# Kernel tuning notes

Measured on AMD Instinct MI355X. Metric: run time of the kernel, lower is better.

Reference implementation:

```python
import jax, jax.numpy as jnp
import numpy as np

ATT_SCALE = 1.0

def setup_inputs() -> dict:
    key = jax.random.key(0)
    ks = jax.random.split(key, 9)
    N, Cin, Cout, E = 50000, 512, 512, 400000
    x = jax.random.normal(ks[0], (N, Cin), dtype=jnp.float32)
    eb = jax.random.randint(ks[1], (2, E), 0, N, dtype=jnp.int32)
    ev = jax.random.randint(ks[2], (2, E), 0, N, dtype=jnp.int32)
    ec = jax.random.randint(ks[3], (2, E), 0, N, dtype=jnp.int32)
    s = 1.0 / np.sqrt(Cin)
    W_bond = jax.random.normal(ks[4], (Cout, Cin), dtype=jnp.float32) * s
    W_vin = jax.random.normal(ks[5], (Cout, Cin), dtype=jnp.float32) * s
    W_vconn = jax.random.normal(ks[6], (Cout, Cin), dtype=jnp.float32) * s
    att_proj = jax.random.normal(ks[7], (Cout,), dtype=jnp.float32)
    bias = jnp.zeros((Cout,), dtype=jnp.float32)
    return {"x": x, "edge_index_bond": eb, "edge_index_virtual_intra": ev,
            "edge_index_virtual_conn": ec, "W_bond": W_bond, "W_vin": W_vin,
            "W_vconn": W_vconn, "att_proj": att_proj, "bias": bias}

def reference(x, edge_index_bond, edge_index_virtual_intra, edge_index_virtual_conn,
              W_bond, W_vin, W_vconn, att_proj, bias):
    N = x.shape[0]
    x_bond = x @ W_bond.T    # [N, Cout]
    x_vin = x @ W_vin.T
    x_vconn = x @ W_vconn.T

    # --- bond edges: add self loops, symmetric degree normalization ---
    loops = jnp.arange(N, dtype=edge_index_bond.dtype)
    row = jnp.concatenate([edge_index_bond[0], loops])
    col = jnp.concatenate([edge_index_bond[1], loops])
    deg = jax.ops.segment_sum(jnp.ones_like(row, dtype=x_bond.dtype), row, num_segments=N)
    dinv = jnp.where(deg > 0, deg ** -0.5, 0.0)
    norm = dinv[row] * dinv[col]                       # [E+N]
    out = jax.ops.segment_sum(x_bond[col] * norm[:, None], row, num_segments=N)

    # --- virtual intra edges: mean aggregation ---
    row_v, col_v = edge_index_virtual_intra[0], edge_index_virtual_intra[1]
    sum_vin = jax.ops.segment_sum(x_vin[col_v], row_v, num_segments=N)
    deg_vin = jnp.clip(jax.ops.segment_sum(jnp.ones_like(row_v, dtype=x_vin.dtype), row_v, num_segments=N), 1.0)
    out = out + sum_vin / deg_vin[:, None]

    # --- virtual conn edges: sigmoid dot-product attention ---
    row_c, col_c = edge_index_virtual_conn[0], edge_index_virtual_conn[1]
    proj_i = x_vconn[row_c] * att_proj
    proj_j = x_vconn[col_c] * att_proj
    alpha = jax.nn.sigmoid(jnp.sum(proj_i * proj_j, axis=-1) * ATT_SCALE)  # [E]
    out = out + jax.ops.segment_sum(alpha[:, None] * x_vconn[col_c], row_c, num_segments=N)

    return out + bias
```

## Files before the change

kernel.cpp:

```cpp
#include <hip/hip_runtime.h>
#include <hip/hip_fp8.h>
#include <stdint.h>

typedef _Float16 f16x8 __attribute__((ext_vector_type(8)));
typedef _Float16 f16x2 __attribute__((ext_vector_type(2)));
typedef float f32x4 __attribute__((ext_vector_type(4)));
typedef float f32x2 __attribute__((ext_vector_type(2)));

__device__ __forceinline__ unsigned short f2h(float f) {
    _Float16 h = (_Float16)f;
    return __builtin_bit_cast(unsigned short, h);
}
__device__ __forceinline__ float h2f(unsigned short s) {
    _Float16 h = __builtin_bit_cast(_Float16, s);
    return (float)h;
}

__device__ __forceinline__ unsigned pack_q4(float f0, float f1, float f2, float f3) {
#if __has_builtin(__builtin_amdgcn_cvt_pk_fp8_f32)
    unsigned u = (unsigned)__builtin_amdgcn_cvt_pk_fp8_f32(f0, f1, 0, false);
    u = (unsigned)__builtin_amdgcn_cvt_pk_fp8_f32(f2, f3, u, true);
    return u;
#else
    __hip_fp8_e4m3 q0(f0), q1(f1), q2(f2), q3(f3);
    return (unsigned)q0.__x | ((unsigned)q1.__x << 8) |
           ((unsigned)q2.__x << 16) | ((unsigned)q3.__x << 24);
#endif
}
__device__ __forceinline__ void add_q8(float* a, uint2 v, float s) {
#if __has_builtin(__builtin_amdgcn_cvt_pk_f32_fp8)
    f32x2 p0 = __builtin_amdgcn_cvt_pk_f32_fp8(v.x, false);
    f32x2 p1 = __builtin_amdgcn_cvt_pk_f32_fp8(v.x, true);
    f32x2 p2 = __builtin_amdgcn_cvt_pk_f32_fp8(v.y, false);
    f32x2 p3 = __builtin_amdgcn_cvt_pk_f32_fp8(v.y, true);
    a[0] += s * p0[0]; a[1] += s * p0[1];
    a[2] += s * p1[0]; a[3] += s * p1[1];
    a[4] += s * p2[0]; a[5] += s * p2[1];
    a[6] += s * p3[0]; a[7] += s * p3[1];
#else
    unsigned char b[8];
    *(uint2*)b = v;
    #pragma unroll
    for (int j = 0; j < 8; j++) {
        __hip_fp8_e4m3 q; q.__x = b[j];
        a[j] += s * (float)q;
    }
#endif
}

__device__ __forceinline__ void gload16(const void* g, void* lds) {
    __builtin_amdgcn_global_load_lds(
        (const __attribute__((address_space(1))) void*)g,
        (__attribute__((address_space(3))) void*)lds, 16, 0, 0);
}

#if __has_builtin(__builtin_amdgcn_fdot2)
__device__ __forceinline__ float dot2(f16x2 a, f16x2 b, float c) {
    return __builtin_amdgcn_fdot2(a, b, c, false);
}
#else
__device__ __forceinline__ float dot2(f16x2 a, f16x2 b, float c) {
    return c + (float)a[0] * (float)b[0] + (float)a[1] * (float)b[1];
}
#endif

__global__ __launch_bounds__(256) void k_prep(
    const float* __restrict__ x, unsigned short* __restrict__ xf,
    size_t valid, size_t total,
    const float* __restrict__ Wb, const float* __restrict__ Wv,
    const float* __restrict__ Wc, unsigned short* __restrict__ Wf,
    const int* __restrict__ eb, const int* __restrict__ ev, const int* __restrict__ ec,
    int Eb, int Ev, int Ec, int* __restrict__ cnt, int N)
{
    size_t i = (size_t)blockIdx.x * 256 + threadIdx.x;
    size_t idx = i * 4;
    if (idx < total) {
        ushort4 h;
        if (idx < valid) {
            float4 f = *(const float4*)(x + idx);
            h.x = f2h(f.x); h.y = f2h(f.y); h.z = f2h(f.z); h.w = f2h(f.w);
        } else {
            h.x = h.y = h.z = h.w = 0;
        }
        *(ushort4*)(xf + idx) = h;
    }
    if (idx < (size_t)1536 * 512) {
        int m = (int)(idx >> 9), k = (int)(idx & 511);
        const float* src;
        if (m < 512)       src = Wb + (size_t)m * 512 + k;
        else if (m < 1024) src = Wv + (size_t)(m - 512) * 512 + k;
        else               src = Wc + (size_t)(m - 1024) * 512 + k;
        float4 f = *(const float4*)src;
        ushort4 h;
        h.x = f2h(f.x); h.y = f2h(f.y); h.z = f2h(f.z); h.w = f2h(f.w);
        *(ushort4*)(Wf + idx) = h;
    }
    if (i < (size_t)(Eb + Ev + Ec)) {
        int ii = (int)i;
        if (ii < Eb) atomicAdd(cnt + eb[ii], 1);
        else if (ii < Eb + Ev) atomicAdd(cnt + N + ev[ii - Eb], 1);
        else atomicAdd(cnt + 2 * N + ec[ii - Eb - Ev], 1);
    }
}

__global__ __launch_bounds__(256) void k_scan_a(
    const int* __restrict__ cnt, int* __restrict__ ptr, int* __restrict__ bsum, int M)
{
    __shared__ int sh[256];
    int t = threadIdx.x;
    int base = blockIdx.x * 1024 + t * 4;
    int v[4];
    #pragma unroll
    for (int j = 0; j < 4; j++) v[j] = (base + j < M) ? cnt[base + j] : 0;
    int local = v[0] + v[1] + v[2] + v[3];
    sh[t] = local; __syncthreads();
    #pragma unroll
    for (int off = 1; off < 256; off <<= 1) {
        int x = (t >= off) ? sh[t - off] : 0;
        __syncthreads();
        sh[t] += x;
        __syncthreads();
    }
    int run = sh[t] - local;
    #pragma unroll
    for (int j = 0; j < 4; j++) {
        if (base + j < M) ptr[base + j] = run;
        run += v[j];
    }
    if (t == 255) bsum[blockIdx.x] = sh[255];
}

__global__ __launch_bounds__(256) void k_scan_c(
    int* __restrict__ ptr, const int* __restrict__ bsum, int* __restrict__ cur,
    const int* __restrict__ cnt, float* __restrict__ dinv,
    int M, int N, int total, int nb)
{
    __shared__ int raw[256], scn[256];
    int t = threadIdx.x;
    int v = (t < nb) ? bsum[t] : 0;
    raw[t] = v; scn[t] = v; __syncthreads();
    #pragma unroll
    for (int off = 1; off < 256; off <<= 1) {
        int x = (t >= off) ? scn[t - off] : 0;
        __syncthreads();
        scn[t] += x;
        __syncthreads();
    }
    int idx = blockIdx.x * 256 + t;
    if (idx < M) {
        int blk = idx >> 10;
        int p = ptr[idx] + (scn[blk] - raw[blk]);
        ptr[idx] = p;
        cur[idx] = p;
        if (idx < N) dinv[idx] = rsqrtf((float)(cnt[idx] + 1));
    }
    if (idx == 0) ptr[M] = total;
}

__global__ __launch_bounds__(256) void k_scatter3(
    const int* __restrict__ eb, const int* __restrict__ ev, const int* __restrict__ ec,
    int Eb, int Ev, int Ec, int* __restrict__ cur, int* __restrict__ cidx, int N)
{
    int i = blockIdx.x * 256 + threadIdx.x;
    const int* e; int il, off, E;
    if (i < Eb) { e = eb; il = i; off = 0; E = Eb; }
    else if (i < Eb + Ev) { e = ev; il = i - Eb; off = N; E = Ev; }
    else if (i < Eb + Ev + Ec) { e = ec; il = i - Eb - Ev; off = 2 * N; E = Ec; }
    else return;
    int r = e[il], c = e[E + il];
    int pos = atomicAdd(cur + off + r, 1);
    cidx[pos] = c;
}

__global__ __launch_bounds__(256) void k_gemm_f(
    const unsigned short* __restrict__ xf, const unsigned short* __restrict__ Wf,
    const float* __restrict__ dinv, int N,
    unsigned char* __restrict__ Ybv, unsigned short* __restrict__ Ycf)
{
    __shared__ uint4 As[2][1024];
    __shared__ uint4 Bs[2][1024];

    const int id = blockIdx.x;
    const int xcd = id & 7;
    const int jj = id >> 3;
    const int bn = jj % 12;
    const int bm = xcd + 8 * (jj / 12);

    const int t = threadIdx.x;
    const int lane = t & 63;
    const int w = t >> 6;
    const int wr = w >> 1;
    const int wc = w & 1;
    const int rA = lane >> 3;
    const int cs = lane & 7;

    f32x4 acc[4][4];
    #pragma unroll
    for (int i = 0; i < 4; i++)
        #pragma unroll
        for (int j = 0; j < 4; j++) acc[i][j] = (f32x4){0.f, 0.f, 0.f, 0.f};

    const size_t baseA = (size_t)bm * 128 * 512;
    const size_t baseB = (size_t)bn * 128 * 512;
    const int cg = cs ^ rA;

    #pragma unroll
    for (int j = 0; j < 4; j++) {
        int seg = w * 4 + j;
        int r = seg * 8 + rA;
        gload16(xf + baseA + (size_t)r * 512 + cg * 8, &As[0][seg * 64]);
        gload16(Wf + baseB + (size_t)r * 512 + cg * 8, &Bs[0][seg * 64]);
    }

    int cur = 0;
    for (int step = 0; step < 8; ++step) {
        if (step < 7) {
            int kt = (step + 1) * 64;
            #pragma unroll
            for (int j = 0; j < 4; j++) {
                int seg = w * 4 + j;
                int r = seg * 8 + rA;
                gload16(xf + baseA + (size_t)r * 512 + kt + cg * 8, &As[cur ^ 1][seg * 64]);
                gload16(Wf + baseB + (size_t)r * 512 + kt + cg * 8, &Bs[cur ^ 1][seg * 64]);
            }
            asm volatile("s_waitcnt vmcnt(8)" ::: "memory");
        } else {
            asm volatile("s_waitcnt vmcnt(0)" ::: "memory");
        }
        __builtin_amdgcn_sched_barrier(0);
        __builtin_amdgcn_s_barrier();

        #pragma unroll
        for (int kk = 0; kk < 2; kk++) {
            f16x8 a[4], b[4];
            #pragma unroll
            for (int ni = 0; ni < 4; ni++) {
                int ar = wr * 64 + ni * 16 + (lane & 15);
                int k8 = kk * 4 + (lane >> 4);
                a[ni] = __builtin_bit_cast(f16x8, As[cur][ar * 8 + (k8 ^ (ar & 7))]);
            }
            #pragma unroll
            for (int mi = 0; mi < 4; mi++) {
                int br = wc * 64 + mi * 16 + (lane & 15);
                int k8 = kk * 4 + (lane >> 4);
                b[mi] = __builtin_bit_cast(f16x8, Bs[cur][br * 8 + (k8 ^ (br & 7))]);
            }
            #pragma unroll
            for (int mi = 0; mi < 4; mi++)
                #pragma unroll
                for (int ni = 0; ni < 4; ni++)
                    acc[mi][ni] = __builtin_amdgcn_mfma_f32_16x16x32_f16(
                        b[mi], a[ni], acc[mi][ni], 0, 0, 0);
        }
        asm volatile("s_waitcnt lgkmcnt(0)" ::: "memory");
        __builtin_amdgcn_sched_barrier(0);
        __builtin_amdgcn_s_barrier();
        cur ^= 1;
    }

    const int nbase = bm * 128 + wr * 64 + (lane & 15);
    const int mq = wc * 64 + (lane >> 4) * 4;
    if (bn < 4) {
        #pragma unroll
        for (int ni = 0; ni < 4; ni++) {
            int n = nbase + ni * 16;
            float dv = (n < N) ? dinv[n] : 0.f;
            #pragma unroll
            for (int mi = 0; mi < 4; mi++) {
                int m0 = bn * 128 + mq + mi * 16;
                unsigned u = pack_q4(acc[mi][ni][0] * dv, acc[mi][ni][1] * dv,
                                     acc[mi][ni][2] * dv, acc[mi][ni][3] * dv);
                *(unsigned*)(Ybv + (size_t)n * 1024 + m0) = u;
            }
        }
    } else if (bn < 8) {
        #pragma unroll
        for (int ni = 0; ni < 4; ni++) {
            int n = nbase + ni * 16;
            #pragma unroll
            for (int mi = 0; mi < 4; mi++) {
                int m0 = bn * 128 + mq + mi * 16;
                unsigned u = pack_q4(acc[mi][ni][0], acc[mi][ni][1],
                                     acc[mi][ni][2], acc[mi][ni][3]);
                *(unsigned*)(Ybv + (size_t)n * 1024 + m0) = u;
            }
        }
    } else {
        #pragma unroll
        for (int ni = 0; ni < 4; ni++) {
            int n = nbase + ni * 16;
            #pragma unroll
            for (int mi = 0; mi < 4; mi++) {
                int m0 = (bn - 8) * 128 + mq + mi * 16;
                ushort4 h;
                h.x = f2h(acc[mi][ni][0]); h.y = f2h(acc[mi][ni][1]);
                h.z = f2h(acc[mi][ni][2]); h.w = f2h(acc[mi][ni][3]);
                *(ushort4*)(Ycf + (size_t)n * 512 + m0) = h;
            }
        }
    }
}

__device__ __forceinline__ void acc_h8(float* a, uint4 v, float s) {
    a[0] += s * h2f((unsigned short)(v.x & 0xffff));
    a[1] += s * h2f((unsigned short)(v.x >> 16));
    a[2] += s * h2f((unsigned short)(v.y & 0xffff));
    a[3] += s * h2f((unsigned short)(v.y >> 16));
    a[4] += s * h2f((unsigned short)(v.z & 0xffff));
    a[5] += s * h2f((unsigned short)(v.z >> 16));
    a[6] += s * h2f((unsigned short)(v.w & 0xffff));
    a[7] += s * h2f((unsigned short)(v.w >> 16));
}
__device__ __forceinline__ float dot8(const f16x2* ph, uint4 u) {
    float d = 0.f;
    d = dot2(ph[0], __builtin_bit_cast(f16x2, u.x), d);
    d = dot2(ph[1], __builtin_bit_cast(f16x2, u.y), d);
    d = dot2(ph[2], __builtin_bit_cast(f16x2, u.z), d);
    d = dot2(ph[3], __builtin_bit_cast(f16x2, u.w), d);
    return d;
}

__global__ __launch_bounds__(256) void k_gather(
    const int* __restrict__ ptr, const int* __restrict__ cidx,
    const float* __restrict__ dinv,
    const unsigned char* __restrict__ Ybv, const unsigned short* __restrict__ Ycf,
    const float* __restrict__ att, const float* __restrict__ bias,
    float* __restrict__ out, int N)
{
    int node = blockIdx.x * 4 + (threadIdx.x >> 6);
    if (node >= N) return;
    int lane = threadIdx.x & 63;

    float di = dinv[node];
    float a[8] = {0.f, 0.f, 0.f, 0.f, 0.f, 0.f, 0.f, 0.f};

    {
        uint2 v = *((const uint2*)(Ybv + (size_t)node * 1024) + lane);
        add_q8(a, v, 1.0f);
    }
    {
        int e0 = ptr[node], e1 = ptr[node + 1];
        int e = e0;
        for (; e + 4 <= e1; e += 4) {
            int c0 = cidx[e], c1 = cidx[e + 1], c2 = cidx[e + 2], c3 = cidx[e + 3];
            uint2 v0 = *((const uint2*)(Ybv + (size_t)c0 * 1024) + lane);
            uint2 v1 = *((const uint2*)(Ybv + (size_t)c1 * 1024) + lane);
            uint2 v2 = *((const uint2*)(Ybv + (size_t)c2 * 1024) + lane);
            uint2 v3 = *((const uint2*)(Ybv + (size_t)c3 * 1024) + lane);
            add_q8(a, v0, 1.0f); add_q8(a, v1, 1.0f);
            add_q8(a, v2, 1.0f); add_q8(a, v3, 1.0f);
        }
        for (; e < e1; ++e) {
            int c = cidx[e];
            uint2 v = *((const uint2*)(Ybv + (size_t)c * 1024) + lane);
            add_q8(a, v, 1.0f);
        }
    }
    {
        const float4* bp = (const float4*)(bias + lane * 8);
        float4 q0 = bp[0], q1 = bp[1];
        a[0] = a[0] * di + q0.x; a[1] = a[1] * di + q0.y;
        a[2] = a[2] * di + q0.z; a[3] = a[3] * di + q0.w;
        a[4] = a[4] * di + q1.x; a[5] = a[5] * di + q1.y;
        a[6] = a[6] * di + q1.z; a[7] = a[7] * di + q1.w;
    }
    {
        int e0 = ptr[N + node], e1 = ptr[N + node + 1];
        float vsc = 1.0f / (float)((e1 - e0) > 1 ? (e1 - e0) : 1);
        int e = e0;
        for (; e + 4 <= e1; e += 4) {
            int c0 = cidx[e], c1 = cidx[e + 1], c2 = cidx[e + 2], c3 = cidx[e + 3];
            uint2 v0 = *((const uint2*)(Ybv + (size_t)c0 * 1024 + 512) + lane);
            uint2 v1 = *((const uint2*)(Ybv + (size_t)c1 * 1024 + 512) + lane);
            uint2 v2 = *((const uint2*)(Ybv + (size_t)c2 * 1024 + 512) + lane);
            uint2 v3 = *((const uint2*)(Ybv + (size_t)c3 * 1024 + 512) + lane);
            add_q8(a, v0, vsc); add_q8(a, v1, vsc);
            add_q8(a, v2, vsc); add_q8(a, v3, vsc);
        }
        for (; e < e1; ++e) {
            int c = cidx[e];
            uint2 v = *((const uint2*)(Ybv + (size_t)c * 1024 + 512) + lane);
            add_q8(a, v, vsc);
        }
    }
    {
        int e0 = ptr[2 * N + node], e1 = ptr[2 * N + node + 1];
        if (e0 < e1) {
            const float4* ap = (const float4*)att + lane * 2;
            float4 t0 = ap[0], t1 = ap[1];
            float yr[8];
            {
                uint4 u = *((const uint4*)(Ycf + (size_t)node * 512) + lane);
                yr[0] = h2f((unsigned short)(u.x & 0xffff));
                yr[1] = h2f((unsigned short)(u.x >> 16));
                yr[2] = h2f((unsigned short)(u.y & 0xffff));
                yr[3] = h2f((unsigned short)(u.y >> 16));
                yr[4] = h2f((unsigned short)(u.z & 0xffff));
                yr[5] = h2f((unsigned short)(u.z >> 16));
                yr[6] = h2f((unsigned short)(u.w & 0xffff));
                yr[7] = h2f((unsigned short)(u.w >> 16));
            }
            f16x2 ph[4];
            ph[0] = (f16x2){(_Float16)(yr[0] * t0.x * t0.x), (_Float16)(yr[1] * t0.y * t0.y)};
            ph[1] = (f16x2){(_Float16)(yr[2] * t0.z * t0.z), (_Float16)(yr[3] * t0.w * t0.w)};
            ph[2] = (f16x2){(_Float16)(yr[4] * t1.x * t1.x), (_Float16)(yr[5] * t1.y * t1.y)};
            ph[3] = (f16x2){(_Float16)(yr[6] * t1.z * t1.z), (_Float16)(yr[7] * t1.w * t1.w)};
            int e = e0;
            for (; e + 4 <= e1; e += 4) {
                int c0 = cidx[e], c1 = cidx[e + 1], c2 = cidx[e + 2], c3 = cidx[e + 3];
                uint4 u0 = *((const uint4*)(Ycf + (size_t)c0 * 512) + lane);
                uint4 u1 = *((const uint4*)(Ycf + (size_t)c1 * 512) + lane);
                uint4 u2 = *((const uint4*)(Ycf + (size_t)c2 * 512) + lane);
                uint4 u3 = *((const uint4*)(Ycf + (size_t)c3 * 512) + lane);
                float d0 = dot8(ph, u0);
                float d1 = dot8(ph, u1);
                float d2 = dot8(ph, u2);
                float d3 = dot8(ph, u3);
                #pragma unroll
                for (int off = 32; off > 0; off >>= 1) {
                    d0 += __shfl_xor(d0, off);
                    d1 += __shfl_xor(d1, off);
                    d2 += __shfl_xor(d2, off);
                    d3 += __shfl_xor(d3, off);
                }
                float al0 = 1.0f / (1.0f + __expf(-d0));
                float al1 = 1.0f / (1.0f + __expf(-d1));
                float al2 = 1.0f / (1.0f + __expf(-d2));
                float al3 = 1.0f / (1.0f + __expf(-d3));
                acc_h8(a, u0, al0); acc_h8(a, u1, al1);
                acc_h8(a, u2, al2); acc_h8(a, u3, al3);
            }
            for (; e < e1; ++e) {
                int c = cidx[e];
                uint4 u = *((const uint4*)(Ycf + (size_t)c * 512) + lane);
                float dot = dot8(ph, u);
                #pragma unroll
                for (int off = 32; off > 0; off >>= 1) dot += __shfl_xor(dot, off);
                float alpha = 1.0f / (1.0f + __expf(-dot));
                acc_h8(a, u, alpha);
            }
        }
    }
    f32x4 o0 = (f32x4){a[0], a[1], a[2], a[3]};
    f32x4 o1 = (f32x4){a[4], a[5], a[6], a[7]};
    f32x4* dst = (f32x4*)(out + (size_t)node * 512 + lane * 8);
    __builtin_nontemporal_store(o0, dst);
    __builtin_nontemporal_store(o1, dst + 1);
}

extern "C" void kernel_launch(void* const* d_in, const int* in_sizes, int n_in,
                              void* d_out, int out_size, void* d_ws, size_t ws_size,
                              hipStream_t stream) {
    const float* x    = (const float*)d_in[0];
    const int*   eb   = (const int*)d_in[1];
    const int*   ev   = (const int*)d_in[2];
    const int*   ec   = (const int*)d_in[3];
    const float* Wb   = (const float*)d_in[4];
    const float* Wv   = (const float*)d_in[5];
    const float* Wc   = (const float*)d_in[6];
    const float* att  = (const float*)d_in[7];
    const float* bias = (const float*)d_in[8];
    float* out = (float*)d_out;

    const int N  = in_sizes[0] / 512;
    const int Eb = in_sizes[1] / 2;
    const int Ev = in_sizes[2] / 2;
    const int Ec = in_sizes[3] / 2;
    const int Etot = Eb + Ev + Ec;
    const int nbm = (((N + 127) / 128 + 7) / 8) * 8;
    const size_t Npad = (size_t)nbm * 128;
    const int M = 3 * N;
    const int nScanBlocks = (M + 1023) / 1024;

    char* p = (char*)d_ws;
    unsigned char*  Ybv = (unsigned char*)p;  p += Npad * 1024;
    unsigned short* Ycf = (unsigned short*)p; p += Npad * 512 * 2;
    unsigned short* Wf  = (unsigned short*)p; p += (size_t)1536 * 512 * 2;
    unsigned short* xf  = (unsigned short*)p; p += Npad * 512 * 2;
    int* cnt  = (int*)p; p += ((size_t)M * 4 + 255) & ~(size_t)255;
    int* ptr_ = (int*)p; p += ((size_t)(M + 1) * 4 + 255) & ~(size_t)255;
    int* cur  = (int*)p; p += ((size_t)M * 4 + 255) & ~(size_t)255;
    int* bsum = (int*)p; p += 256 * 4;
    int* cidx = (int*)p; p += ((size_t)Etot * 4 + 255) & ~(size_t)255;
    float* dinv = (float*)p; p += ((size_t)N * 4 + 255) & ~(size_t)255;

    const size_t total = Npad * 512, valid = (size_t)N * 512;

    hipMemsetAsync(cnt, 0, (size_t)M * 4, stream);
    k_prep<<<(int)((total / 4 + 255) / 256), 256, 0, stream>>>(
        x, xf, valid, total, Wb, Wv, Wc, Wf, eb, ev, ec, Eb, Ev, Ec, cnt, N);

    k_scan_a<<<nScanBlocks, 256, 0, stream>>>(cnt, ptr_, bsum, M);
    k_scan_c<<<(M + 255) / 256, 256, 0, stream>>>(ptr_, bsum, cur, cnt, dinv, M, N, Etot, nScanBlocks);
    k_scatter3<<<(Etot + 255) / 256, 256, 0, stream>>>(eb, ev, ec, Eb, Ev, Ec, cur, cidx, N);

    k_gemm_f<<<nbm * 12, 256, 0, stream>>>(xf, Wf, dinv, N, Ybv, Ycf);

    k_gather<<<(N + 3) / 4, 256, 0, stream>>>(ptr_, cidx, dinv, Ybv, Ycf, att, bias, out, N);
}
```

Before: 394.0 us.

## Fuse CSR build into one cooperative kernel and interleave bond/vin gathers

Merges the prep, two-stage scan, and scatter kernels into a single cooperative kernel that uses grid-wide syncs, with the old four-launch path kept as a fallback. The aim is to remove the launch gaps between the small preprocessing kernels. The gather kernel now loads bond and virtual-intra neighbours in the same loop into separate accumulators, which raises memory-level parallelism, and applies both scales at the end. The cost is a fixed 1024-block grid, serialized grid.sync phases, and more registers per thread in the gather.

Measured after the change: 745.6 us. 1.89x slower.

```diff
diff --git a/kernel.cpp b/kernel.cpp
--- a/kernel.cpp
+++ b/kernel.cpp
@@ -1,6 +1,9 @@
 #include <hip/hip_runtime.h>
+#include <hip/hip_cooperative_groups.h>
 #include <hip/hip_fp8.h>
 #include <stdint.h>
+
+namespace cg = cooperative_groups;
 
 typedef _Float16 f16x8 __attribute__((ext_vector_type(8)));
 typedef _Float16 f16x2 __attribute__((ext_vector_type(2)));
@@ -27,23 +30,23 @@
            ((unsigned)q2.__x << 16) | ((unsigned)q3.__x << 24);
 #endif
 }
-__device__ __forceinline__ void add_q8(float* a, uint2 v, float s) {
+__device__ __forceinline__ void add_q8a(float* a, uint2 v) {
 #if __has_builtin(__builtin_amdgcn_cvt_pk_f32_fp8)
     f32x2 p0 = __builtin_amdgcn_cvt_pk_f32_fp8(v.x, false);
     f32x2 p1 = __builtin_amdgcn_cvt_pk_f32_fp8(v.x, true);
     f32x2 p2 = __builtin_amdgcn_cvt_pk_f32_fp8(v.y, false);
     f32x2 p3 = __builtin_amdgcn_cvt_pk_f32_fp8(v.y, true);
-    a[0] += s * p0[0]; a[1] += s * p0[1];
-    a[2] += s * p1[0]; a[3] += s * p1[1];
-    a[4] += s * p2[0]; a[5] += s * p2[1];
-    a[6] += s * p3[0]; a[7] += s * p3[1];
+    a[0] += p0[0]; a[1] += p0[1];
+    a[2] += p1[0]; a[3] += p1[1];
+    a[4] += p2[0]; a[5] += p2[1];
+    a[6] += p3[0]; a[7] += p3[1];
 #else
     unsigned char b[8];
     *(uint2*)b = v;
     #pragma unroll
     for (int j = 0; j < 8; j++) {
         __hip_fp8_e4m3 q; q.__x = b[j];
-        a[j] += s * (float)q;
+        a[j] += (float)q;
     }
 #endif
 }
@@ -63,6 +66,113 @@
     return c + (float)a[0] * (float)b[0] + (float)a[1] * (float)b[1];
 }
 #endif
+
+__global__ __launch_bounds__(256) void k_build(
+    const float* __restrict__ x, unsigned short* __restrict__ xf,
+    size_t valid, size_t total,
+    const float* __restrict__ Wb, const float* __restrict__ Wv,
+    const float* __restrict__ Wc, unsigned short* __restrict__ Wf,
+    const int* __restrict__ eb, const int* __restrict__ ev, const int* __restrict__ ec,
+    int Eb, int Ev, int Ec,
+    int* __restrict__ cnt, int* __restrict__ ptr, int* __restrict__ bsum,
+    int* __restrict__ cur, int* __restrict__ cidx, float* __restrict__ dinv,
+    int M, int N, int totalE)
+{
+    cg::grid_group grid = cg::this_grid();
+    const int t = threadIdx.x;
+    const int gsz = (int)gridDim.x;
+    __shared__ int sh[256];
+    __shared__ int raw[256], scn[256];
+    const int Etot = Eb + Ev + Ec;
+
+    size_t nquad = total >> 2;
+    for (size_t i = (size_t)blockIdx.x * 256 + t; i < nquad; i += (size_t)gsz * 256) {
+        size_t idx = i * 4;
+        ushort4 h;
+        if (idx < valid) {
+            float4 f = *(const float4*)(x + idx);
+            h.x = f2h(f.x); h.y = f2h(f.y); h.z = f2h(f.z); h.w = f2h(f.w);
+        } else {
+            h.x = h.y = h.z = h.w = 0;
+        }
+        *(ushort4*)(xf + idx) = h;
+    }
+    for (size_t i = (size_t)blockIdx.x * 256 + t; i < (size_t)196608; i += (size_t)gsz * 256) {
+        size_t idx = i * 4;
+        int m = (int)(idx >> 9), k = (int)(idx & 511);
+        const float* src;
+        if (m < 512)       src = Wb + (size_t)m * 512 + k;
+        else if (m < 1024) src = Wv + (size_t)(m - 512) * 512 + k;
+        else               src = Wc + (size_t)(m - 1024) * 512 + k;
+        float4 f = *(const float4*)src;
+        ushort4 h;
+        h.x = f2h(f.x); h.y = f2h(f.y); h.z = f2h(f.z); h.w = f2h(f.w);
+        *(ushort4*)(Wf + idx) = h;
+    }
+    for (int i = blockIdx.x * 256 + t; i < Etot; i += gsz * 256) {
+        if (i < Eb) atomicAdd(cnt + eb[i], 1);
+        else if (i < Eb + Ev) atomicAdd(cnt + N + ev[i - Eb], 1);
+        else atomicAdd(cnt + 2 * N + ec[i - Eb - Ev], 1);
+    }
+    grid.sync();
+
+    const int nScan = (M + 1023) >> 10;
+    for (int c = blockIdx.x; c < nScan; c += gsz) {
+        int base = c * 1024 + t * 4;
+        int v[4];
+        #pragma unroll
+        for (int j = 0; j < 4; j++) v[j] = (base + j < M) ? cnt[base + j] : 0;
+        int local = v[0] + v[1] + v[2] + v[3];
+        __syncthreads();
+        sh[t] = local; __syncthreads();
+        #pragma unroll
+        for (int off = 1; off < 256; off <<= 1) {
+            int xv = (t >= off) ? sh[t - off] : 0;
+            __syncthreads();
+            sh[t] += xv;
+            __syncthreads();
+        }
+        int run = sh[t] - local;
+        #pragma unroll
+        for (int j = 0; j < 4; j++) {
+            if (base + j < M) ptr[base + j] = run;
+            run += v[j];
+        }
+        if (t == 255) bsum[c] = sh[255];
+    }
+    grid.sync();
+
+    {
+        int v = (t < nScan) ? bsum[t] : 0;
+        raw[t] = v; scn[t] = v; __syncthreads();
+        #pragma unroll
+        for (int off = 1; off < 256; off <<= 1) {
+            int xv = (t >= off) ? scn[t - off] : 0;
+            __syncthreads();
+            scn[t] += xv;
+            __syncthreads();
+        }
+        for (int idx = blockIdx.x * 256 + t; idx < M; idx += gsz * 256) {
+            int blk = idx >> 10;
+            int p = ptr[idx] + (scn[blk] - raw[blk]);
+            ptr[idx] = p;
+            cur[idx] = p;
+            if (idx < N) dinv[idx] = rsqrtf((float)(cnt[idx] + 1));
+        }
+        if (blockIdx.x == 0 && t == 0) ptr[M] = totalE;
+    }
+    grid.sync();
+
+    for (int i = blockIdx.x * 256 + t; i < Etot; i += gsz * 256) {
+        const int* e; int il, off, E;
+        if (i < Eb) { e = eb; il = i; off = 0; E = Eb; }
+        else if (i < Eb + Ev) { e = ev; il = i - Eb; off = N; E = Ev; }
+        else { e = ec; il = i - Eb - Ev; off = 2 * N; E = Ec; }
+        int r = e[il], c = e[E + il];
+        int pos = atomicAdd(cur + off + r, 1);
+        cidx[pos] = c;
+    }
+}
 
 __global__ __launch_bounds__(256) void k_prep(
     const float* __restrict__ x, unsigned short* __restrict__ xf,
@@ -202,14 +312,14 @@
 
     const size_t baseA = (size_t)bm * 128 * 512;
     const size_t baseB = (size_t)bn * 128 * 512;
-    const int cg = cs ^ rA;
+    const int cg_ = cs ^ rA;
 
     #pragma unroll
     for (int j = 0; j < 4; j++) {
         int seg = w * 4 + j;
         int r = seg * 8 + rA;
-        gload16(xf + baseA + (size_t)r * 512 + cg * 8, &As[0][seg * 64]);
-        gload16(Wf + baseB + (size_t)r * 512 + cg * 8, &Bs[0][seg * 64]);
+        gload16(xf + baseA + (size_t)r * 512 + cg_ * 8, &As[0][seg * 64]);
+        gload16(Wf + baseB + (size_t)r * 512 + cg_ * 8, &Bs[0][seg * 64]);
     }
 
     int cur = 0;
@@ -220,8 +330,8 @@
             for (int j = 0; j < 4; j++) {
                 int seg = w * 4 + j;
                 int r = seg * 8 + rA;
-                gload16(xf + baseA + (size_t)r * 512 + kt + cg * 8, &As[cur ^ 1][seg * 64]);
-                gload16(Wf + baseB + (size_t)r * 512 + kt + cg * 8, &Bs[cur ^ 1][seg * 64]);
+                gload16(xf + baseA + (size_t)r * 512 + kt + cg_ * 8, &As[cur ^ 1][seg * 64]);
+                gload16(Wf + baseB + (size_t)r * 512 + kt + cg_ * 8, &Bs[cur ^ 1][seg * 64]);
             }
             asm volatile("s_waitcnt vmcnt(8)" ::: "memory");
         } else {
@@ -332,57 +442,71 @@
     int lane = threadIdx.x & 63;
 
     float di = dinv[node];
-    float a[8] = {0.f, 0.f, 0.f, 0.f, 0.f, 0.f, 0.f, 0.f};
+    float ab[8] = {0.f, 0.f, 0.f, 0.f, 0.f, 0.f, 0.f, 0.f};
+    float av[8] = {0.f, 0.f, 0.f, 0.f, 0.f, 0.f, 0.f, 0.f};
 
     {
         uint2 v = *((const uint2*)(Ybv + (size_t)node * 1024) + lane);
-        add_q8(a, v, 1.0f);
-    }
-    {
-        int e0 = ptr[node], e1 = ptr[node + 1];
-        int e = e0;
-        for (; e + 4 <= e1; e += 4) {
-            int c0 = cidx[e], c1 = cidx[e + 1], c2 = cidx[e + 2], c3 = cidx[e + 3];
-            uint2 v0 = *((const uint2*)(Ybv + (size_t)c0 * 1024) + lane);
-            uint2 v1 = *((const uint2*)(Ybv + (size_t)c1 * 1024) + lane);
-            uint2 v2 = *((const uint2*)(Ybv + (size_t)c2 * 1024) + lane);
-            uint2 v3 = *((const uint2*)(Ybv + (size_t)c3 * 1024) + lane);
-            add_q8(a, v0, 1.0f); add_q8(a, v1, 1.0f);
-            add_q8(a, v2, 1.0f); add_q8(a, v3, 1.0f);
-        }
-        for (; e < e1; ++e) {
-            int c = cidx[e];
-            uint2 v = *((const uint2*)(Ybv + (size_t)c * 1024) + lane);
-            add_q8(a, v, 1.0f);
-        }
-    }
+        add_q8a(ab, v);
+    }
+    int eb = ptr[node], eb1 = ptr[node + 1];
+    int ev = ptr[N + node], ev1 = ptr[N + node + 1];
+    float vsc = 1.0f / (float)((ev1 - ev) > 1 ? (ev1 - ev) : 1);
+
+    while (eb + 4 <= eb1 && ev + 4 <= ev1) {
+        int b0 = cidx[eb], b1 = cidx[eb + 1], b2 = cidx[eb + 2], b3 = cidx[eb + 3];
+        int c0 = cidx[ev], c1 = cidx[ev + 1], c2 = cidx[ev + 2], c3 = cidx[ev + 3];
+        uint2 B0 = *((const uint2*)(Ybv + (size_t)b0 * 1024) + lane);
+        uint2 B1 = *((const uint2*)(Ybv + (size_t)b1 * 1024) + lane);
+        uint2 B2 = *((const uint2*)(Ybv + (size_t)b2 * 1024) + lane);
+        uint2 B3 = *((const uint2*)(Ybv + (size_t)b3 * 1024) + lane);
+        uint2 V0 = *((const uint2*)(Ybv + (size_t)c0 * 1024 + 512) + lane);
+        uint2 V1 = *((const uint2*)(Ybv + (size_t)c1 * 1024 + 512) + lane);
+        uint2 V2 = *((const uint2*)(Ybv + (size_t)c2 * 1024 + 512) + lane);
+        uint2 V3 = *((const uint2*)(Ybv + (size_t)c3 * 1024 + 512) + lane);
+        add_q8a(ab, B0); add_q8a(ab, B1); add_q8a(ab, B2); add_q8a(ab, B3);
+        add_q8a(av, V0); add_q8a(av, V1); add_q8a(av, V2); add_q8a(av, V3);
+        eb += 4; ev += 4;
+    }
+    for (; eb + 4 <= eb1; eb += 4) {
+        int b0 = cidx[eb], b1 = cidx[eb + 1], b2 = cidx[eb + 2], b3 = cidx[eb + 3];
+        uint2 B0 = *((const uint2*)(Ybv + (size_t)b0 * 1024) + lane);
+        uint2 B1 = *((const uint2*)(Ybv + (size_t)b1 * 1024) + lane);
+        uint2 B2 = *((const uint2*)(Ybv + (size_t)b2 * 1024) + lane);
+        uint2 B3 = *((const uint2*)(Ybv + (size_t)b3 * 1024) + lane);
+        add_q8a(ab, B0); add_q8a(ab, B1); add_q8a(ab, B2); add_q8a(ab, B3);
+    }
+    for (; eb < eb1; ++eb) {
+        uint2 v = *((const uint2*)(Ybv + (size_t)cidx[eb] * 1024) + lane);
+        add_q8a(ab, v);
+    }
+    for (; ev + 4 <= ev1; ev += 4) {
+        int c0 = cidx[ev], c1 = cidx[ev + 1], c2 = cidx[ev + 2], c3 = cidx[ev + 3];
+        uint2 V0 = *((const uint2*)(Ybv + (size_t)c0 * 1024 + 512) + lane);
+        uint2 V1 = *((const uint2*)(Ybv + (size_t)c1 * 1024 + 512) + lane);
+        uint2 V2 = *((const uint2*)(Ybv + (size_t)c2 * 1024 + 512) + lane);
+        uint2 V3 = *((const uint2*)(Ybv + (size_t)c3 * 1024 + 512) + lane);
+        add_q8a(av, V0); add_q8a(av, V1); add_q8a(av, V2); add_q8a(av, V3);
+    }
+    for (; ev < ev1; ++ev) {
+        uint2 v = *((const uint2*)(Ybv + (size_t)cidx[ev] * 1024 + 512) + lane);
+        add_q8a(av, v);
+    }
+
+    float a[8];
     {
         const float4* bp = (const float4*)(bias + lane * 8);
         float4 q0 = bp[0], q1 = bp[1];
-        a[0] = a[0] * di + q0.x; a[1] = a[1] * di + q0.y;
-        a[2] = a[2] * di + q0.z; a[3] = a[3] * di + q0.w;
-        a[4] = a[4] * di + q1.x; a[5] = a[5] * di + q1.y;
-        a[6] = a[6] * di + q1.z; a[7] = a[7] * di + q1.w;
-    }
-    {
-        int e0 = ptr[N + node], e1 = ptr[N + node + 1];
-        float vsc = 1.0f / (float)((e1 - e0) > 1 ? (e1 - e0) : 1);
-        int e = e0;
-        for (; e + 4 <= e1; e += 4) {
-            int c0 = cidx[e], c1 = cidx[e + 1], c2 = cidx[e + 2], c3 = cidx[e + 3];
-            uint2 v0 = *((const uint2*)(Ybv + (size_t)c0 * 1024 + 512) + lane);
-            uint2 v1 = *((const uint2*)(Ybv + (size_t)c1 * 1024 + 512) + lane);
-            uint2 v2 = *((const uint2*)(Ybv + (size_t)c2 * 1024 + 512) + lane);
-            uint2 v3 = *((const uint2*)(Ybv + (size_t)c3 * 1024 + 512) + lane);
-            add_q8(a, v0, vsc); add_q8(a, v1, vsc);
-            add_q8(a, v2, vsc); add_q8(a, v3, vsc);
-        }
-        for (; e < e1; ++e) {
-            int c = cidx[e];
-            uint2 v = *((const uint2*)(Ybv + (size_t)c * 1024 + 512) + lane);
-            add_q8(a, v, vsc);
-        }
-    }
+        a[0] = ab[0] * di + av[0] * vsc + q0.x;
+        a[1] = ab[1] * di + av[1] * vsc + q0.y;
+        a[2] = ab[2] * di + av[2] * vsc + q0.z;
+        a[3] = ab[3] * di + av[3] * vsc + q0.w;
+        a[4] = ab[4] * di + av[4] * vsc + q1.x;
+        a[5] = ab[5] * di + av[5] * vsc + q1.y;
+        a[6] = ab[6] * di + av[6] * vsc + q1.z;
+        a[7] = ab[7] * di + av[7] * vsc + q1.w;
+    }
+
     {
         int e0 = ptr[2 * N + node], e1 = ptr[2 * N + node + 1];
         if (e0 < e1) {
@@ -484,15 +608,29 @@
     int* cidx = (int*)p; p += ((size_t)Etot * 4 + 255) & ~(size_t)255;
     float* dinv = (float*)p; p += ((size_t)N * 4 + 255) & ~(size_t)255;
 
-    const size_t total = Npad * 512, valid = (size_t)N * 512;
+    size_t total = Npad * 512, valid = (size_t)N * 512;
 
     hipMemsetAsync(cnt, 0, (size_t)M * 4, stream);
-    k_prep<<<(int)((total / 4 + 255) / 256), 256, 0, stream>>>(
-        x, xf, valid, total, Wb, Wv, Wc, Wf, eb, ev, ec, Eb, Ev, Ec, cnt, N);
-
-    k_scan_a<<<nScanBlocks, 256, 0, stream>>>(cnt, ptr_, bsum, M);
-    k_scan_c<<<(M + 255) / 256, 256, 0, stream>>>(ptr_, bsum, cur, cnt, dinv, M, N, Etot, nScanBlocks);
-    k_scatter3<<<(Etot + 255) / 256, 256, 0, stream>>>(eb, ev, ec, Eb, Ev, Ec, cur, cidx, N);
+
+    int Mv = M, Nv = N, EtotV = Etot;
+    int Ebv = Eb, Evv = Ev, Ecv = Ec;
+    void* kargs[] = {
+        (void*)&x, (void*)&xf, (void*)&valid, (void*)&total,
+        (void*)&Wb, (void*)&Wv, (void*)&Wc, (void*)&Wf,
+        (void*)&eb, (void*)&ev, (void*)&ec,
+        (void*)&Ebv, (void*)&Evv, (void*)&Ecv,
+        (void*)&cnt, (void*)&ptr_, (void*)&bsum, (void*)&cur, (void*)&cidx, (void*)&dinv,
+        (void*)&Mv, (void*)&Nv, (void*)&EtotV
+    };
+    hipError_t cerr = hipLaunchCooperativeKernel(
+        (void*)k_build, dim3(1024), dim3(256), kargs, 0, stream);
+    if (cerr != hipSuccess) {
+        k_prep<<<(int)((total / 4 + 255) / 256), 256, 0, stream>>>(
+            x, xf, valid, total, Wb, Wv, Wc, Wf, eb, ev, ec, Eb, Ev, Ec, cnt, N);
+        k_scan_a<<<nScanBlocks, 256, 0, stream>>>(cnt, ptr_, bsum, M);
+        k_scan_c<<<(M + 255) / 256, 256, 0, stream>>>(ptr_, bsum, cur, cnt, dinv, M, N, Etot, nScanBlocks);
+        k_scatter3<<<(Etot + 255) / 256, 256, 0, stream>>>(eb, ev, ec, Eb, Ev, Ec, cur, cidx, N);
+    }
 
     k_gemm_f<<<nbm * 12, 256, 0, stream>>>(xf, Wf, dinv, N, Ybv, Ycf);
 
```
